# Performance work log

Hardware: AMD Instinct MI355X
Metric: run time of the kernel (lower is better)

Reference implementation:

```python
import jax, jax.numpy as jnp
import numpy as np

B, T, C = 4, 2048, 1024
N_HEAD = 16
HEAD = C // N_HEAD

def setup_inputs() -> dict:
    key = jax.random.key(0)
    k1, k2, k3 = jax.random.split(key, 3)
    x = jax.random.normal(k1, (B, T, C), dtype=jnp.float32)
    w_attn = jax.random.normal(k2, (C, 3 * C), dtype=jnp.float32) * (1.0 / np.sqrt(C))
    w_proj = jax.random.normal(k3, (C, C), dtype=jnp.float32) * (1.0 / np.sqrt(C))
    return {"x": x, "w_attn": w_attn, "w_proj": w_proj}

def reference(x, w_attn, w_proj):
    b, t, c = x.shape
    qkv = x @ w_attn  # [B,T,3C]
    q, k, v = jnp.split(qkv, 3, axis=-1)
    # [B,T,C] -> [B,H,T,D]
    def heads(z):
        return z.reshape(b, t, N_HEAD, HEAD).transpose(0, 2, 1, 3)
    q, k, v = heads(q), heads(k), heads(v)
    scale = 1.0 / np.sqrt(HEAD)
    att = jnp.einsum('bhqd,bhkd->bhqk', q, k) * scale  # [B,H,T,T]
    causal = jnp.tril(jnp.ones((t, t), dtype=bool))
    att = jnp.where(causal[None, None], att, -jnp.inf)
    att = jax.nn.softmax(att, axis=-1)
    y = jnp.einsum('bhqk,bhkd->bhqd', att, v)  # [B,H,T,D]
    y = y.transpose(0, 2, 1, 3).reshape(b, t, c)
    return y @ w_proj
```

## Files before the change

### kernel.cpp

```cpp
#include <hip/hip_runtime.h>
#include <hip/hip_bf16.h>


typedef __attribute__((ext_vector_type(8))) short bf16x8;
typedef __attribute__((ext_vector_type(4))) float f32x4;
typedef __attribute__((ext_vector_type(16))) float f32x16;

#define T_DIM 2048
#define NHEAD 16
#define HDIM  64

__device__ __forceinline__ unsigned short f2bf(float f) {
    union { float f; unsigned int u; } v; v.f = f;
    unsigned int r = v.u + 0x7fffu + ((v.u >> 16) & 1u);
    return (unsigned short)(r >> 16);
}

__device__ __forceinline__ unsigned cvtpk_bf16(float lo, float hi) {
    unsigned r;
    asm("v_cvt_pk_bf16_f32 %0, %1, %2" : "=v"(r) : "v"(lo), "v"(hi));
    return r;
}
__device__ __forceinline__ void pl32swap(unsigned &x, unsigned &y) {
    asm("v_permlane32_swap_b32 %0, %1" : "+v"(x), "+v"(y));
}
__device__ __forceinline__ bf16x8 mk8(unsigned w0, unsigned w1, unsigned w2, unsigned w3) {
    union { unsigned u[4]; bf16x8 v; } p;
    p.u[0] = w0; p.u[1] = w1; p.u[2] = w2; p.u[3] = w3;
    return p.v;
}

__device__ __forceinline__ void gload_lds16(const void* g, void* l) {
    __builtin_amdgcn_global_load_lds(
        (const __attribute__((address_space(1))) void*)g,
        (__attribute__((address_space(3))) void*)l,
        16, 0, 0);
}

__global__ void cvt_bf16_k(const float* __restrict__ src, unsigned short* __restrict__ dst, int n) {
    int i = (blockIdx.x * blockDim.x + threadIdx.x) * 4;
    if (i < n) {
        float4 v = *(const float4*)(src + i);
        ushort4 o; o.x = f2bf(v.x); o.y = f2bf(v.y); o.z = f2bf(v.z); o.w = f2bf(v.w);
        *(ushort4*)(dst + i) = o;
    }
}

__global__ void transpose_wb_k(const float* __restrict__ src, unsigned short* __restrict__ dst,
                               int R, int Cc) {
    __shared__ float tile[32][33];
    int c0 = blockIdx.x * 32, r0 = blockIdx.y * 32;
    int tx = threadIdx.x & 31, ty = threadIdx.x >> 5;
    #pragma unroll
    for (int i = 0; i < 32; i += 8)
        tile[ty + i][tx] = src[(size_t)(r0 + ty + i) * Cc + c0 + tx];
    __syncthreads();
    #pragma unroll
    for (int i = 0; i < 32; i += 8)
        dst[(size_t)(c0 + ty + i) * R + r0 + tx] = f2bf(tile[tx][ty + i]);
}

template<int EPI>
__global__ __launch_bounds__(256) void gemm_bt_k(
    const unsigned short* __restrict__ A, const unsigned short* __restrict__ Bt,
    void* __restrict__ out0, void* __restrict__ out1, void* __restrict__ out2,
    int M, int N, int K)
{
    __shared__ __align__(16) unsigned short smem[16384];
    unsigned short* sA = smem;
    unsigned short* sB = smem + 8192;

    const int tid = threadIdx.x, lane = tid & 63, wave = tid >> 6;
    const int wm = wave >> 1, wn = wave & 1;
    const int lrow = lane & 15, hi = lane >> 4;

    const int nwg = gridDim.x * gridDim.y;
    const int lin = blockIdx.y * gridDim.x + blockIdx.x;
    const int lin2 = (lin & 7) * (nwg >> 3) + (lin >> 3);
    const int bxg = lin2 % gridDim.x, byg = lin2 / gridDim.x;
    const int row0 = byg * 128, col0 = bxg * 128;

    const int arow = tid >> 3;
    const int gk = ((tid & 7) ^ (arow & 7)) * 8;
    const unsigned short* gA = A  + (size_t)(row0 + arow) * K + gk;
    const unsigned short* gB = Bt + (size_t)(col0 + arow) * K + gk;

    const int NT = K >> 6;

#define STAGE(t) { const size_t ko_ = (size_t)(t) * 64; \
        gload_lds16(gA + ko_,                   sA + tid * 8); \
        gload_lds16(gA + (size_t)32 * K + ko_,  sA + (tid + 256) * 8); \
        gload_lds16(gA + (size_t)64 * K + ko_,  sA + (tid + 512) * 8); \
        gload_lds16(gA + (size_t)96 * K + ko_,  sA + (tid + 768) * 8); \
        gload_lds16(gB + ko_,                   sB + tid * 8); \
        gload_lds16(gB + (size_t)32 * K + ko_,  sB + (tid + 256) * 8); \
        gload_lds16(gB + (size_t)64 * K + ko_,  sB + (tid + 512) * 8); \
        gload_lds16(gB + (size_t)96 * K + ko_,  sB + (tid + 768) * 8); }

    f32x4 acc[4][4] = {};

    for (int t = 0; t < NT; ++t) {
        STAGE(t);
        __syncthreads();
        bf16x8 af[2][4], bf_[2][4];
        #pragma unroll
        for (int ks = 0; ks < 2; ++ks) {
            const int kc = (ks * 4 + hi) ^ (lrow & 7);
            #pragma unroll
            for (int mi = 0; mi < 4; ++mi)
                af[ks][mi] = *(const bf16x8*)&sA[((wm * 64 + mi * 16 + lrow) * 8 + kc) * 8];
            #pragma unroll
            for (int ni = 0; ni < 4; ++ni)
                bf_[ks][ni] = *(const bf16x8*)&sB[((wn * 64 + ni * 16 + lrow) * 8 + kc) * 8];
        }
        __builtin_amdgcn_s_setprio(1);
        #pragma unroll
        for (int ks = 0; ks < 2; ++ks)
            #pragma unroll
            for (int mi = 0; mi < 4; ++mi)
                #pragma unroll
                for (int ni = 0; ni < 4; ++ni)
                    acc[mi][ni] = __builtin_amdgcn_mfma_f32_16x16x32_bf16(af[ks][mi], bf_[ks][ni], acc[mi][ni], 0, 0, 0);
        __builtin_amdgcn_s_setprio(0);
        __syncthreads();
    }
#undef STAGE

    if (EPI == 1) {
        #pragma unroll
        for (int mi = 0; mi < 4; ++mi)
            #pragma unroll
            for (int ni = 0; ni < 4; ++ni) {
                int gm0 = row0 + wm * 64 + mi * 16 + hi * 4;
                int gn  = col0 + wn * 64 + ni * 16 + lrow;
                #pragma unroll
                for (int r = 0; r < 4; ++r)
                    ((float*)out0)[(size_t)(gm0 + r) * N + gn] = acc[mi][ni][r];
            }
    } else if (col0 < 1024) {
        const int bb = row0 >> 11;
        #pragma unroll
        for (int mi = 0; mi < 4; ++mi)
            #pragma unroll
            for (int ni = 0; ni < 4; ++ni) {
                int gm0 = row0 + wm * 64 + mi * 16 + hi * 4;
                int gn  = col0 + wn * 64 + ni * 16 + lrow;
                int h = (gn >> 6) & 15, d = gn & 63;
                #pragma unroll
                for (int r = 0; r < 4; ++r) {
                    int t = (gm0 + r) & 2047;
                    ((unsigned short*)out0)[((size_t)(bb * NHEAD + h) * T_DIM + t) * HDIM + d] =
                        f2bf(acc[mi][ni][r] * 0.18033688011112042f);
                }
            }
    } else {
        const bool isK = (col0 < 2048);
        __syncthreads();
        #pragma unroll
        for (int mi = 0; mi < 4; ++mi) {
            #pragma unroll
            for (int ni = 0; ni < 4; ++ni) {
                const int gnl = wn * 64 + ni * 16 + lrow;
                const int hl = gnl >> 6, d = gnl & 63;
                #pragma unroll
                for (int r = 0; r < 4; ++r) {
                    const int tl = wm * 64 + mi * 16 + hi * 4 + r;
                    int idx;
                    if (isK) idx = (hl * 2 + (tl >> 6)) * 4096 + ((d >> 3) * 64 + (tl & 63)) * 8 + (d & 7);
                    else     idx = (hl * 2 + (tl >> 6)) * 4096 + (((tl >> 3) & 7) * 64 + d) * 8 + (tl & 7);
                    smem[idx] = f2bf(acc[mi][ni][r]);
                }
            }
        }
        __syncthreads();
        unsigned short* outb = (unsigned short*)(isK ? out1 : out2);
        const int bb = row0 >> 11;
        const int h0 = ((col0 - (isK ? 1024 : 2048)) >> 6);
        const int tc0 = (row0 & 2047) >> 6;
        #pragma unroll
        for (int seg = 0; seg < 4; ++seg) {
            const int hl = seg >> 1, tc = seg & 1;
            const size_t gbase = ((size_t)(bb * NHEAD + h0 + hl) * 32 + tc0 + tc) * 4096;
            *(uint4*)(outb + gbase + tid * 8)         = *(const uint4*)(smem + seg * 4096 + tid * 8);
            *(uint4*)(outb + gbase + (tid + 256) * 8) = *(const uint4*)(smem + seg * 4096 + (tid + 256) * 8);
        }
    }
}

__global__ __launch_bounds__(512) void attn_k(
    const unsigned short* __restrict__ qb, const unsigned short* __restrict__ kcm,
    const unsigned short* __restrict__ vcm, unsigned short* __restrict__ yb)
{
    __shared__ __align__(16) unsigned short Ks[2][4096];
    __shared__ __align__(16) unsigned short Vs[2][4096];

    const int tid = threadIdx.x, lane = tid & 63, wave = tid >> 6;
    const int bh = blockIdx.y;
    const int q32 = lane & 31, hi32 = lane >> 5;
    const unsigned short* Kg = kcm + (size_t)bh * 32 * 4096;
    const unsigned short* Vg = vcm + (size_t)bh * 32 * 4096;

    #pragma unroll
    for (int pass = 0; pass < 2; ++pass) {
        const int bxx = (pass == 0) ? (int)blockIdx.x : (7 - (int)blockIdx.x);
        const int ntiles = 4 * bxx + 4;
        const int q0w = bxx * 256 + wave * 32;
        const int qg = q0w + q32;

        const unsigned short* qrow = qb + ((size_t)bh * T_DIM + q0w + q32) * HDIM;
        bf16x8 qf[4];
        #pragma unroll
        for (int kc = 0; kc < 4; ++kc)
            qf[kc] = *(const bf16x8*)(qrow + kc * 16 + hi32 * 8);

        f32x16 o0 = {}, o1 = {};
        float lsum = 0.f;

        gload_lds16(Kg + tid * 8, &Ks[0][tid * 8]);
        gload_lds16(Vg + tid * 8, &Vs[0][tid * 8]);
        __syncthreads();

        int cur = 0;
        for (int jt = 0; jt < ntiles; ++jt) {
            if (jt + 1 < ntiles) {
                gload_lds16(Kg + (size_t)(jt + 1) * 4096 + tid * 8, &Ks[cur ^ 1][tid * 8]);
                gload_lds16(Vg + (size_t)(jt + 1) * 4096 + tid * 8, &Vs[cur ^ 1][tid * 8]);
            }
            if (jt * 64 <= q0w + 31) {
                f32x16 s0 = {}, s1 = {};
                #pragma unroll
                for (int kc = 0; kc < 4; ++kc) {
                    bf16x8 a0 = *(const bf16x8*)&Ks[cur][((kc * 2 + hi32) * 64 + q32) * 8];
                    bf16x8 a1 = *(const bf16x8*)&Ks[cur][((kc * 2 + hi32) * 64 + 32 + q32) * 8];
                    s0 = __builtin_amdgcn_mfma_f32_32x32x16_bf16(a0, qf[kc], s0, 0, 0, 0);
                    s1 = __builtin_amdgcn_mfma_f32_32x32x16_bf16(a1, qf[kc], s1, 0, 0, 0);
                }
                if (jt * 64 + 63 > q0w) {
                    #pragma unroll
                    for (int r = 0; r < 16; ++r) {
                        int kv0 = jt * 64 + (r & 3) + 8 * (r >> 2) + 4 * hi32;
                        if (kv0 > qg)      s0[r] = -1e30f;
                        if (kv0 + 32 > qg) s1[r] = -1e30f;
                    }
                }
                bf16x8 pa[4];
                #pragma unroll
                for (int blk = 0; blk < 2; ++blk) {
                    float p_[16]; unsigned w_[8];
                    #pragma unroll
                    for (int i = 0; i < 16; ++i) {
                        float sv = blk ? s1[i] : s0[i];
                        p_[i] = __builtin_amdgcn_exp2f(sv - 16.0f);
                        lsum += p_[i];
                    }
                    #pragma unroll
                    for (int i = 0; i < 8; ++i) w_[i] = cvtpk_bf16(p_[2 * i], p_[2 * i + 1]);
                    pl32swap(w_[0], w_[2]); pl32swap(w_[1], w_[3]);
                    pl32swap(w_[4], w_[6]); pl32swap(w_[5], w_[7]);
                    pa[blk * 2]     = mk8(w_[0], w_[1], w_[2], w_[3]);
                    pa[blk * 2 + 1] = mk8(w_[4], w_[5], w_[6], w_[7]);
                }
                #pragma unroll
                for (int kvc = 0; kvc < 4; ++kvc) {
                    bf16x8 b0 = *(const bf16x8*)&Vs[cur][((kvc * 2 + hi32) * 64 + q32) * 8];
                    bf16x8 b1 = *(const bf16x8*)&Vs[cur][((kvc * 2 + hi32) * 64 + 32 + q32) * 8];
                    o0 = __builtin_amdgcn_mfma_f32_32x32x16_bf16(pa[kvc], b0, o0, 0, 0, 0);
                    o1 = __builtin_amdgcn_mfma_f32_32x32x16_bf16(pa[kvc], b1, o1, 0, 0, 0);
                }
            }
            __syncthreads();
            cur ^= 1;
        }

        {
            unsigned la = __float_as_uint(lsum), lb = __float_as_uint(lsum);
            pl32swap(la, lb);
            lsum = __uint_as_float(la) + __uint_as_float(lb);
        }
        const int bb2 = bh >> 4, h = bh & 15;
        #pragma unroll
        for (int r = 0; r < 16; ++r) {
            const int cr = (r & 3) + 8 * (r >> 2) + 4 * hi32;
            float inv = 1.0f / __shfl(lsum, cr);
            int t = q0w + cr;
            size_t off = ((size_t)(bb2 * T_DIM + t)) * 1024 + h * HDIM + q32;
            yb[off]      = f2bf(o0[r] * inv);
            yb[off + 32] = f2bf(o1[r] * inv);
        }
    }
}

extern "C" void kernel_launch(void* const* d_in, const int* in_sizes, int n_in,
                              void* d_out, int out_size, void* d_ws, size_t ws_size,
                              hipStream_t stream) {
    const float* x      = (const float*)d_in[0];
    const float* w_attn = (const float*)d_in[1];
    const float* w_proj = (const float*)d_in[2];
    float* out = (float*)d_out;

    unsigned short* xb  = (unsigned short*)d_ws;
    unsigned short* wat = xb  + (size_t)8192 * 1024;
    unsigned short* wpt = wat + (size_t)3072 * 1024;
    unsigned short* qb  = wpt + (size_t)1024 * 1024;
    unsigned short* kcm = qb  + (size_t)64 * 2048 * 64;
    unsigned short* vcm = kcm + (size_t)64 * 2048 * 64;
    unsigned short* yb  = vcm + (size_t)64 * 2048 * 64;

    cvt_bf16_k<<<8192, 256, 0, stream>>>(x, xb, 8192 * 1024);
    transpose_wb_k<<<dim3(96, 32), 256, 0, stream>>>(w_attn, wat, 1024, 3072);
    transpose_wb_k<<<dim3(32, 32), 256, 0, stream>>>(w_proj, wpt, 1024, 1024);

    gemm_bt_k<0><<<dim3(24, 64), 256, 0, stream>>>(xb, wat, qb, kcm, vcm, 8192, 3072, 1024);
    attn_k<<<dim3(4, 64), 512, 0, stream>>>(qb, kcm, vcm, yb);
    gemm_bt_k<1><<<dim3(8, 64), 256, 0, stream>>>(yb, wpt, out, nullptr, nullptr, 8192, 1024, 1024);
}
```

Baseline: 166.5 us.

## Split long causal attention rows across blocks and combine partials in new kernel

Replaces the paired two-pass attention blocks with 768 independent blocks. Each of the four heaviest query tiles is split into two KV ranges whose bf16 partial outputs and row sums go to scratch space, then a new combine kernel sums and normalises them. The aim is better load balance and more parallelism across CUs in exchange for an extra launch, extra global traffic, and bf16 rounding of the unnormalised partials. Scratch memory reuses the xb and wat buffers, which are dead after the QKV GEMM.

```diff
diff --git a/kernel.cpp b/kernel.cpp
--- a/kernel.cpp
+++ b/kernel.cpp
@@ -189,94 +189,102 @@
 
 __global__ __launch_bounds__(512) void attn_k(
     const unsigned short* __restrict__ qb, const unsigned short* __restrict__ kcm,
-    const unsigned short* __restrict__ vcm, unsigned short* __restrict__ yb)
+    const unsigned short* __restrict__ vcm, unsigned short* __restrict__ yb,
+    unsigned short* __restrict__ pob, float* __restrict__ lpart)
 {
     __shared__ __align__(16) unsigned short Ks[2][4096];
     __shared__ __align__(16) unsigned short Vs[2][4096];
 
     const int tid = threadIdx.x, lane = tid & 63, wave = tid >> 6;
-    const int bh = blockIdx.y;
+    const int L = (int)blockIdx.x;
+    const int j = L >> 3;
+    const int bh = (j / 12) * 8 + (L & 7);
+    const int slot = j % 12;
+    int bx, jt0, jt1;
+    if (slot < 4)      { bx = slot;      jt0 = 0;          jt1 = 4 * bx + 4; }
+    else if (slot < 8) { bx = 11 - slot; jt0 = 0;          jt1 = 2 * bx + 2; }
+    else               { bx = 15 - slot; jt0 = 2 * bx + 2; jt1 = 4 * bx + 4; }
+    const bool split = (slot >= 4);
+    const int pidx = (bh * 4 + (bx - 4)) * 2 + (slot >= 8 ? 1 : 0);
+
     const int q32 = lane & 31, hi32 = lane >> 5;
     const unsigned short* Kg = kcm + (size_t)bh * 32 * 4096;
     const unsigned short* Vg = vcm + (size_t)bh * 32 * 4096;
 
+    const int q0w = bx * 256 + wave * 32;
+    const int qg = q0w + q32;
+
+    const unsigned short* qrow = qb + ((size_t)bh * T_DIM + q0w + q32) * HDIM;
+    bf16x8 qf[4];
     #pragma unroll
-    for (int pass = 0; pass < 2; ++pass) {
-        const int bxx = (pass == 0) ? (int)blockIdx.x : (7 - (int)blockIdx.x);
-        const int ntiles = 4 * bxx + 4;
-        const int q0w = bxx * 256 + wave * 32;
-        const int qg = q0w + q32;
-
-        const unsigned short* qrow = qb + ((size_t)bh * T_DIM + q0w + q32) * HDIM;
-        bf16x8 qf[4];
-        #pragma unroll
-        for (int kc = 0; kc < 4; ++kc)
-            qf[kc] = *(const bf16x8*)(qrow + kc * 16 + hi32 * 8);
-
-        f32x16 o0 = {}, o1 = {};
-        float lsum = 0.f;
-
-        gload_lds16(Kg + tid * 8, &Ks[0][tid * 8]);
-        gload_lds16(Vg + tid * 8, &Vs[0][tid * 8]);
-        __syncthreads();
-
-        int cur = 0;
-        for (int jt = 0; jt < ntiles; ++jt) {
-            if (jt + 1 < ntiles) {
-                gload_lds16(Kg + (size_t)(jt + 1) * 4096 + tid * 8, &Ks[cur ^ 1][tid * 8]);
-                gload_lds16(Vg + (size_t)(jt + 1) * 4096 + tid * 8, &Vs[cur ^ 1][tid * 8]);
-            }
-            if (jt * 64 <= q0w + 31) {
-                f32x16 s0 = {}, s1 = {};
-                #pragma unroll
-                for (int kc = 0; kc < 4; ++kc) {
-                    bf16x8 a0 = *(const bf16x8*)&Ks[cur][((kc * 2 + hi32) * 64 + q32) * 8];
-                    bf16x8 a1 = *(const bf16x8*)&Ks[cur][((kc * 2 + hi32) * 64 + 32 + q32) * 8];
-                    s0 = __builtin_amdgcn_mfma_f32_32x32x16_bf16(a0, qf[kc], s0, 0, 0, 0);
-                    s1 = __builtin_amdgcn_mfma_f32_32x32x16_bf16(a1, qf[kc], s1, 0, 0, 0);
+    for (int kc = 0; kc < 4; ++kc)
+        qf[kc] = *(const bf16x8*)(qrow + kc * 16 + hi32 * 8);
+
+    f32x16 o0 = {}, o1 = {};
+    float lsum = 0.f;
+
+    gload_lds16(Kg + (size_t)jt0 * 4096 + tid * 8, &Ks[0][tid * 8]);
+    gload_lds16(Vg + (size_t)jt0 * 4096 + tid * 8, &Vs[0][tid * 8]);
+    __syncthreads();
+
+    int cur = 0;
+    for (int jt = jt0; jt < jt1; ++jt) {
+        if (jt + 1 < jt1) {
+            gload_lds16(Kg + (size_t)(jt + 1) * 4096 + tid * 8, &Ks[cur ^ 1][tid * 8]);
+            gload_lds16(Vg + (size_t)(jt + 1) * 4096 + tid * 8, &Vs[cur ^ 1][tid * 8]);
+        }
+        if (jt * 64 <= q0w + 31) {
+            f32x16 s0 = {}, s1 = {};
+            #pragma unroll
+            for (int kc = 0; kc < 4; ++kc) {
+                bf16x8 a0 = *(const bf16x8*)&Ks[cur][((kc * 2 + hi32) * 64 + q32) * 8];
+                bf16x8 a1 = *(const bf16x8*)&Ks[cur][((kc * 2 + hi32) * 64 + 32 + q32) * 8];
+                s0 = __builtin_amdgcn_mfma_f32_32x32x16_bf16(a0, qf[kc], s0, 0, 0, 0);
+                s1 = __builtin_amdgcn_mfma_f32_32x32x16_bf16(a1, qf[kc], s1, 0, 0, 0);
+            }
+            if (jt * 64 + 63 > q0w) {
+                #pragma unroll
+                for (int r = 0; r < 16; ++r) {
+                    int kv0 = jt * 64 + (r & 3) + 8 * (r >> 2) + 4 * hi32;
+                    if (kv0 > qg)      s0[r] = -1e30f;
+                    if (kv0 + 32 > qg) s1[r] = -1e30f;
                 }
-                if (jt * 64 + 63 > q0w) {
-                    #pragma unroll
-                    for (int r = 0; r < 16; ++r) {
-                        int kv0 = jt * 64 + (r & 3) + 8 * (r >> 2) + 4 * hi32;
-                        if (kv0 > qg)      s0[r] = -1e30f;
-                        if (kv0 + 32 > qg) s1[r] = -1e30f;
-                    }
+            }
+            bf16x8 pa[4];
+            #pragma unroll
+            for (int blk = 0; blk < 2; ++blk) {
+                float p_[16]; unsigned w_[8];
+                #pragma unroll
+                for (int i = 0; i < 16; ++i) {
+                    float sv = blk ? s1[i] : s0[i];
+                    p_[i] = __builtin_amdgcn_exp2f(sv - 16.0f);
+                    lsum += p_[i];
                 }
-                bf16x8 pa[4];
-                #pragma unroll
-                for (int blk = 0; blk < 2; ++blk) {
-                    float p_[16]; unsigned w_[8];
-                    #pragma unroll
-                    for (int i = 0; i < 16; ++i) {
-                        float sv = blk ? s1[i] : s0[i];
-                        p_[i] = __builtin_amdgcn_exp2f(sv - 16.0f);
-                        lsum += p_[i];
-                    }
-                    #pragma unroll
-                    for (int i = 0; i < 8; ++i) w_[i] = cvtpk_bf16(p_[2 * i], p_[2 * i + 1]);
-                    pl32swap(w_[0], w_[2]); pl32swap(w_[1], w_[3]);
-                    pl32swap(w_[4], w_[6]); pl32swap(w_[5], w_[7]);
-                    pa[blk * 2]     = mk8(w_[0], w_[1], w_[2], w_[3]);
-                    pa[blk * 2 + 1] = mk8(w_[4], w_[5], w_[6], w_[7]);
-                }
-                #pragma unroll
-                for (int kvc = 0; kvc < 4; ++kvc) {
-                    bf16x8 b0 = *(const bf16x8*)&Vs[cur][((kvc * 2 + hi32) * 64 + q32) * 8];
-                    bf16x8 b1 = *(const bf16x8*)&Vs[cur][((kvc * 2 + hi32) * 64 + 32 + q32) * 8];
-                    o0 = __builtin_amdgcn_mfma_f32_32x32x16_bf16(pa[kvc], b0, o0, 0, 0, 0);
-                    o1 = __builtin_amdgcn_mfma_f32_32x32x16_bf16(pa[kvc], b1, o1, 0, 0, 0);
-                }
-            }
-            __syncthreads();
-            cur ^= 1;
-        }
-
-        {
-            unsigned la = __float_as_uint(lsum), lb = __float_as_uint(lsum);
-            pl32swap(la, lb);
-            lsum = __uint_as_float(la) + __uint_as_float(lb);
-        }
+                #pragma unroll
+                for (int i = 0; i < 8; ++i) w_[i] = cvtpk_bf16(p_[2 * i], p_[2 * i + 1]);
+                pl32swap(w_[0], w_[2]); pl32swap(w_[1], w_[3]);
+                pl32swap(w_[4], w_[6]); pl32swap(w_[5], w_[7]);
+                pa[blk * 2]     = mk8(w_[0], w_[1], w_[2], w_[3]);
+                pa[blk * 2 + 1] = mk8(w_[4], w_[5], w_[6], w_[7]);
+            }
+            #pragma unroll
+            for (int kvc = 0; kvc < 4; ++kvc) {
+                bf16x8 b0 = *(const bf16x8*)&Vs[cur][((kvc * 2 + hi32) * 64 + q32) * 8];
+                bf16x8 b1 = *(const bf16x8*)&Vs[cur][((kvc * 2 + hi32) * 64 + 32 + q32) * 8];
+                o0 = __builtin_amdgcn_mfma_f32_32x32x16_bf16(pa[kvc], b0, o0, 0, 0, 0);
+                o1 = __builtin_amdgcn_mfma_f32_32x32x16_bf16(pa[kvc], b1, o1, 0, 0, 0);
+            }
+        }
+        __syncthreads();
+        cur ^= 1;
+    }
+
+    {
+        unsigned la = __float_as_uint(lsum), lb = __float_as_uint(lsum);
+        pl32swap(la, lb);
+        lsum = __uint_as_float(la) + __uint_as_float(lb);
+    }
+    if (!split) {
         const int bb2 = bh >> 4, h = bh & 15;
         #pragma unroll
         for (int r = 0; r < 16; ++r) {
@@ -287,6 +295,44 @@
             yb[off]      = f2bf(o0[r] * inv);
             yb[off + 32] = f2bf(o1[r] * inv);
         }
+    } else {
+        if (hi32 == 0) lpart[pidx * 256 + wave * 32 + q32] = lsum;
+        unsigned short* po = pob + (size_t)pidx * 16384;
+        #pragma unroll
+        for (int r = 0; r < 16; ++r) {
+            const int cr = (r & 3) + 8 * (r >> 2) + 4 * hi32;
+            int row = wave * 32 + cr;
+            po[row * 64 + q32]      = f2bf(o0[r]);
+            po[row * 64 + 32 + q32] = f2bf(o1[r]);
+        }
+    }
+}
+
+__global__ __launch_bounds__(256) void combine_k(const unsigned short* __restrict__ pob,
+                                                 const float* __restrict__ lpart,
+                                                 unsigned short* __restrict__ yb) {
+    const int blk = blockIdx.x;
+    const int bh = blk >> 2, bx = (blk & 3) + 4;
+    const int row = threadIdx.x;
+    const int p0i = blk * 2;
+    const int t = bx * 256 + row;
+    const float inv = 1.0f / (lpart[p0i * 256 + row] + lpart[(p0i + 1) * 256 + row]);
+    const unsigned short* p0 = pob + (size_t)p0i * 16384 + row * 64;
+    const unsigned short* p1 = p0 + 16384;
+    const int bb = bh >> 4, h = bh & 15;
+    unsigned short* y = yb + ((size_t)(bb * T_DIM + t)) * 1024 + h * HDIM;
+    #pragma unroll
+    for (int c = 0; c < 8; ++c) {
+        union { uint4 u; unsigned short s[8]; } a, b, o;
+        a.u = *(const uint4*)(p0 + c * 8);
+        b.u = *(const uint4*)(p1 + c * 8);
+        #pragma unroll
+        for (int jj = 0; jj < 8; ++jj) {
+            float fa = __uint_as_float((unsigned)a.s[jj] << 16);
+            float fb = __uint_as_float((unsigned)b.s[jj] << 16);
+            o.s[jj] = f2bf((fa + fb) * inv);
+        }
+        *(uint4*)(y + c * 8) = o.u;
     }
 }
 
@@ -305,12 +351,15 @@
     unsigned short* kcm = qb  + (size_t)64 * 2048 * 64;
     unsigned short* vcm = kcm + (size_t)64 * 2048 * 64;
     unsigned short* yb  = vcm + (size_t)64 * 2048 * 64;
+    unsigned short* pob = xb;
+    float* lpart = (float*)wat;
 
     cvt_bf16_k<<<8192, 256, 0, stream>>>(x, xb, 8192 * 1024);
     transpose_wb_k<<<dim3(96, 32), 256, 0, stream>>>(w_attn, wat, 1024, 3072);
     transpose_wb_k<<<dim3(32, 32), 256, 0, stream>>>(w_proj, wpt, 1024, 1024);
 
     gemm_bt_k<0><<<dim3(24, 64), 256, 0, stream>>>(xb, wat, qb, kcm, vcm, 8192, 3072, 1024);
-    attn_k<<<dim3(4, 64), 512, 0, stream>>>(qb, kcm, vcm, yb);
+    attn_k<<<768, 512, 0, stream>>>(qb, kcm, vcm, yb, pob, lpart);
+    combine_k<<<256, 256, 0, stream>>>(pob, lpart, yb);
     gemm_bt_k<1><<<dim3(8, 64), 256, 0, stream>>>(yb, wpt, out, nullptr, nullptr, 8192, 1024, 1024);
 }
```

Result: slower. 182.4 us (+9.6%).
